# Kernel tuning notes

Measured on AMD Instinct MI355X. Metric: run time of the kernel, lower is better.

The kernel has to match this reference:

```python
import jax, jax.numpy as jnp
import numpy as np

N_NODES = 100000
N_EDGES = 800000
N_GRAPHS = 256
IN_C = 96
HID = 96
OUT_C = 16


def setup_inputs() -> dict:
    key = jax.random.key(0)
    ks = jax.random.split(key, 10)
    x = jax.random.normal(ks[0], (N_NODES, IN_C), dtype=jnp.float32)
    edge_index = jax.random.randint(ks[1], (2, N_EDGES), 0, N_NODES, dtype=jnp.int64)
    batch = jnp.sort(jax.random.randint(ks[2], (N_NODES,), 0, N_GRAPHS, dtype=jnp.int64))
    def glorot(k, fan_in, fan_out):
        s = np.sqrt(6.0 / (fan_in + fan_out)).astype(np.float32)
        return jax.random.uniform(k, (fan_in, fan_out), minval=-s, maxval=s, dtype=jnp.float32)
    W1 = glorot(ks[3], IN_C, HID)
    W2 = glorot(ks[4], HID, HID)
    W3 = glorot(ks[5], HID, HID)
    Wlin = glorot(ks[6], HID, OUT_C)
    b1 = jnp.zeros((HID,), dtype=jnp.float32)
    b2 = jnp.zeros((HID,), dtype=jnp.float32)
    b3 = jnp.zeros((HID,), dtype=jnp.float32)
    return {"x": x, "edge_index": edge_index, "batch": batch,
            "W1": W1, "b1": b1, "W2": W2, "b2": b2, "W3": W3, "b3": b3, "Wlin": Wlin}


def _gcn_conv(x, W, b, src, dst):
    # PyG GCNConv(normalize=True): add self-loops, deg includes self-loop,
    # norm_ij = deg_i^{-1/2} * deg_j^{-1/2}; linear (no bias) then scatter-add; bias after.
    n = x.shape[0]
    deg = jnp.zeros((n,), dtype=x.dtype).at[dst].add(1.0) + 1.0  # +1 self-loop
    dinv = jax.lax.rsqrt(deg)
    h = x @ W                                   # [N, H]
    coef = dinv[src] * dinv[dst]                # [E]
    msg = h[src] * coef[:, None]                # [E, H] gather
    agg = jax.ops.segment_sum(msg, dst, num_segments=n)  # scatter-add
    agg = agg + h * (dinv * dinv)[:, None]      # self-loop contribution
    return agg + b


def reference(x, edge_index, batch, W1, b1, W2, b2, W3, b3, Wlin):
    src, dst = edge_index[0], edge_index[1]
    h = jax.nn.relu(_gcn_conv(x, W1, b1, src, dst))
    h = jax.nn.relu(_gcn_conv(h, W2, b2, src, dst))
    h = _gcn_conv(h, W3, b3, src, dst)
    # global mean pool over graphs
    sums = jax.ops.segment_sum(h, batch, num_segments=N_GRAPHS)
    counts = jax.ops.segment_sum(jnp.ones((h.shape[0],), dtype=h.dtype), batch, num_segments=N_GRAPHS)
    pooled = sums / jnp.maximum(counts, 1.0)[:, None]
    return pooled @ Wlin
```

## Files before the change

kernel.cpp:

```cpp
#include <hip/hip_runtime.h>

#define NN 100000
#define NE 800000
#define NG 256
#define CH 96
#define OC 16
#define NBLK 391
#define TM 128

typedef __attribute__((ext_vector_type(8))) short bf16x8;
typedef __attribute__((ext_vector_type(4))) float f32x4;

__device__ __forceinline__ unsigned short f2bf(float x) {
    unsigned u = __float_as_uint(x);
    return (unsigned short)((u + 0x7fffu + ((u >> 16) & 1u)) >> 16);
}
__device__ __forceinline__ float bf2f(unsigned short h) {
    return __uint_as_float(((unsigned)h) << 16);
}
__device__ __forceinline__ void split8(const float4 a, const float4 b,
                                       bf16x8& hi, bf16x8& lo) {
    float v[8] = {a.x, a.y, a.z, a.w, b.x, b.y, b.z, b.w};
#pragma unroll
    for (int j = 0; j < 8; j++) {
        unsigned short h = f2bf(v[j]);
        hi[j] = (short)h;
        lo[j] = (short)f2bf(v[j] - bf2f(h));
    }
}
__device__ __forceinline__ float4 us4_to_f4(ushort4 u) {
    return make_float4(bf2f(u.x), bf2f(u.y), bf2f(u.z), bf2f(u.w));
}

__global__ __launch_bounds__(256) void k_hist(const int* __restrict__ dst,
                                              int* __restrict__ cnt,
                                              int* __restrict__ slot,
                                              const float* __restrict__ W1,
                                              const float* __restrict__ W2,
                                              const float* __restrict__ W3,
                                              unsigned short* __restrict__ WH,
                                              unsigned short* __restrict__ WL) {
    int e = blockIdx.x * 256 + threadIdx.x;
    slot[e] = atomicAdd(&cnt[dst[e]], 1);
    if (e < 3 * CH * CH) {
        int w = e / (CH * CH);
        int r = e - w * (CH * CH);
        int k = r / CH;
        int n = r - k * CH;
        const float* Ws = (w == 0) ? W1 : (w == 1) ? W2 : W3;
        float v = Ws[k * CH + n];
        unsigned short h = f2bf(v);
        WH[w * CH * CH + n * CH + k] = h;
        WL[w * CH * CH + n * CH + k] = f2bf(v - bf2f(h));
    }
}

__global__ __launch_bounds__(256) void k_offsets(const int* __restrict__ cnt,
                                                 int* __restrict__ gtot,
                                                 int* __restrict__ off,
                                                 float* __restrict__ dinv,
                                                 const int* __restrict__ batch,
                                                 int* __restrict__ goff) {
    int i = blockIdx.x * 256 + threadIdx.x;
    if (i >= NN) return;
    int c = cnt[i];
    off[i] = atomicAdd(gtot, c);
    dinv[i] = rsqrtf((float)c + 1.0f);
    int b = batch[i];
    int bp = (i > 0) ? batch[i - 1] : -1;
    for (int g = bp + 1; g <= b; g++) goff[g] = i;
    if (i == NN - 1)
        for (int g = b + 1; g <= NG; g++) goff[g] = NN;
}

__global__ __launch_bounds__(256) void k_build(const int* __restrict__ src,
                                               const int* __restrict__ dst,
                                               const int* __restrict__ off,
                                               const int* __restrict__ slot,
                                               const float* __restrict__ dinv,
                                               float2* __restrict__ packed) {
    int e = blockIdx.x * 256 + threadIdx.x;
    int s = src[e];
    int d = dst[e];
    packed[off[d] + slot[e]] = make_float2(__int_as_float(s), dinv[s] * dinv[d]);
}

__global__ __launch_bounds__(256) void k_gemm_f32(const float* __restrict__ X,
                                                  const unsigned short* __restrict__ WH,
                                                  const unsigned short* __restrict__ WL,
                                                  unsigned short* __restrict__ H) {
    __shared__ __align__(16) unsigned short WsH[CH * CH];
    __shared__ __align__(16) unsigned short WsL[CH * CH];

    const int tid = threadIdx.x;
    const int n0 = blockIdx.x * TM;

    {
        const uint4* sH = reinterpret_cast<const uint4*>(WH);
        const uint4* sL = reinterpret_cast<const uint4*>(WL);
        uint4* dH = reinterpret_cast<uint4*>(WsH);
        uint4* dL = reinterpret_cast<uint4*>(WsL);
        for (int i = tid; i < CH * CH / 8; i += 256) {
            dH[i] = sH[i];
            dL[i] = sL[i];
        }
    }
    __syncthreads();

    const int lane = tid & 63;
    const int wave = tid >> 6;
    const int lrow = lane & 15;
    const int quad = lane >> 4;

    const float4* X4 = reinterpret_cast<const float4*>(X);

    f32x4 acc[2][6];
#pragma unroll
    for (int rt = 0; rt < 2; rt++)
#pragma unroll
        for (int ct = 0; ct < 6; ct++) acc[rt][ct] = (f32x4){0.f, 0.f, 0.f, 0.f};

    int arow[2];
#pragma unroll
    for (int rt = 0; rt < 2; rt++)
        arow[rt] = min(n0 + (wave * 2 + rt) * 16 + lrow, NN - 1);

#pragma unroll
    for (int kc = 0; kc < 3; kc++) {
        bf16x8 ahi[2], alo[2];
#pragma unroll
        for (int rt = 0; rt < 2; rt++) {
            int fo = (arow[rt] * CH + kc * 32 + quad * 8) >> 2;
            split8(X4[fo], X4[fo + 1], ahi[rt], alo[rt]);
        }
#pragma unroll
        for (int ct = 0; ct < 6; ct++) {
            int bo = (ct * 16 + lrow) * CH + kc * 32 + quad * 8;
            bf16x8 bhi = *reinterpret_cast<const bf16x8*>(&WsH[bo]);
            bf16x8 blo = *reinterpret_cast<const bf16x8*>(&WsL[bo]);
#pragma unroll
            for (int rt = 0; rt < 2; rt++) {
                acc[rt][ct] = __builtin_amdgcn_mfma_f32_16x16x32_bf16(
                    alo[rt], bhi, acc[rt][ct], 0, 0, 0);
                acc[rt][ct] = __builtin_amdgcn_mfma_f32_16x16x32_bf16(
                    ahi[rt], blo, acc[rt][ct], 0, 0, 0);
                acc[rt][ct] = __builtin_amdgcn_mfma_f32_16x16x32_bf16(
                    ahi[rt], bhi, acc[rt][ct], 0, 0, 0);
            }
        }
    }

#pragma unroll
    for (int rt = 0; rt < 2; rt++) {
        int rbase = n0 + (wave * 2 + rt) * 16 + quad * 4;
#pragma unroll
        for (int ct = 0; ct < 6; ct++) {
            int col = ct * 16 + lrow;
#pragma unroll
            for (int r = 0; r < 4; r++) {
                int row = rbase + r;
                if (row < NN) H[(size_t)row * CH + col] = f2bf(acc[rt][ct][r]);
            }
        }
    }
}

__global__ __launch_bounds__(256) void k_gemm_bf16(const unsigned short* __restrict__ X,
                                                   const unsigned short* __restrict__ WH,
                                                   const unsigned short* __restrict__ WL,
                                                   unsigned short* __restrict__ H) {
    __shared__ __align__(16) unsigned short WsH[CH * CH];
    __shared__ __align__(16) unsigned short WsL[CH * CH];

    const int tid = threadIdx.x;
    const int n0 = blockIdx.x * TM;

    {
        const uint4* sH = reinterpret_cast<const uint4*>(WH);
        const uint4* sL = reinterpret_cast<const uint4*>(WL);
        uint4* dH = reinterpret_cast<uint4*>(WsH);
        uint4* dL = reinterpret_cast<uint4*>(WsL);
        for (int i = tid; i < CH * CH / 8; i += 256) {
            dH[i] = sH[i];
            dL[i] = sL[i];
        }
    }
    __syncthreads();

    const int lane = tid & 63;
    const int wave = tid >> 6;
    const int lrow = lane & 15;
    const int quad = lane >> 4;

    f32x4 acc[2][6];
#pragma unroll
    for (int rt = 0; rt < 2; rt++)
#pragma unroll
        for (int ct = 0; ct < 6; ct++) acc[rt][ct] = (f32x4){0.f, 0.f, 0.f, 0.f};

    int arow[2];
#pragma unroll
    for (int rt = 0; rt < 2; rt++)
        arow[rt] = min(n0 + (wave * 2 + rt) * 16 + lrow, NN - 1);

#pragma unroll
    for (int kc = 0; kc < 3; kc++) {
        bf16x8 ahi[2];
#pragma unroll
        for (int rt = 0; rt < 2; rt++)
            ahi[rt] = *reinterpret_cast<const bf16x8*>(
                &X[(size_t)arow[rt] * CH + kc * 32 + quad * 8]);
#pragma unroll
        for (int ct = 0; ct < 6; ct++) {
            int bo = (ct * 16 + lrow) * CH + kc * 32 + quad * 8;
            bf16x8 bhi = *reinterpret_cast<const bf16x8*>(&WsH[bo]);
            bf16x8 blo = *reinterpret_cast<const bf16x8*>(&WsL[bo]);
#pragma unroll
            for (int rt = 0; rt < 2; rt++) {
                acc[rt][ct] = __builtin_amdgcn_mfma_f32_16x16x32_bf16(
                    ahi[rt], blo, acc[rt][ct], 0, 0, 0);
                acc[rt][ct] = __builtin_amdgcn_mfma_f32_16x16x32_bf16(
                    ahi[rt], bhi, acc[rt][ct], 0, 0, 0);
            }
        }
    }

#pragma unroll
    for (int rt = 0; rt < 2; rt++) {
        int rbase = n0 + (wave * 2 + rt) * 16 + quad * 4;
#pragma unroll
        for (int ct = 0; ct < 6; ct++) {
            int col = ct * 16 + lrow;
#pragma unroll
            for (int r = 0; r < 4; r++) {
                int row = rbase + r;
                if (row < NN) H[(size_t)row * CH + col] = f2bf(acc[rt][ct][r]);
            }
        }
    }
}

template <bool RELU, bool B16OUT>
__global__ __launch_bounds__(256) void k_aggregate(const int* __restrict__ off,
                                                   const int* __restrict__ cnt,
                                                   const float2* __restrict__ packed,
                                                   const float* __restrict__ dinv,
                                                   const float* __restrict__ bias,
                                                   const unsigned short* __restrict__ H,
                                                   void* __restrict__ Bout) {
    int idx = blockIdx.x * 256 + threadIdx.x;
    int n = idx / 24;
    int c4 = idx - n * 24;
    int e0 = off[n];
    int e1 = e0 + cnt[n];

    const ushort4* H4 = reinterpret_cast<const ushort4*>(H);
    float di = dinv[n];
    float d2 = di * di;
    float4 h = us4_to_f4(H4[(size_t)n * 24 + c4]);
    float4 bb = reinterpret_cast<const float4*>(bias)[c4];
    float4 acc = make_float4(h.x * d2 + bb.x, h.y * d2 + bb.y,
                             h.z * d2 + bb.z, h.w * d2 + bb.w);

    int e = e0;
    for (; e + 4 <= e1; e += 4) {
        float2 p0 = packed[e + 0];
        float2 p1 = packed[e + 1];
        float2 p2 = packed[e + 2];
        float2 p3 = packed[e + 3];
        float4 v0 = us4_to_f4(H4[(size_t)__float_as_int(p0.x) * 24 + c4]);
        float4 v1 = us4_to_f4(H4[(size_t)__float_as_int(p1.x) * 24 + c4]);
        float4 v2 = us4_to_f4(H4[(size_t)__float_as_int(p2.x) * 24 + c4]);
        float4 v3 = us4_to_f4(H4[(size_t)__float_as_int(p3.x) * 24 + c4]);
        acc.x += v0.x * p0.y + v1.x * p1.y + v2.x * p2.y + v3.x * p3.y;
        acc.y += v0.y * p0.y + v1.y * p1.y + v2.y * p2.y + v3.y * p3.y;
        acc.z += v0.z * p0.y + v1.z * p1.y + v2.z * p2.y + v3.z * p3.y;
        acc.w += v0.w * p0.y + v1.w * p1.y + v2.w * p2.y + v3.w * p3.y;
    }
    for (; e < e1; e++) {
        float2 pc = packed[e];
        float4 v = us4_to_f4(H4[(size_t)__float_as_int(pc.x) * 24 + c4]);
        acc.x += v.x * pc.y; acc.y += v.y * pc.y;
        acc.z += v.z * pc.y; acc.w += v.w * pc.y;
    }
    if (RELU) {
        acc.x = fmaxf(acc.x, 0.0f); acc.y = fmaxf(acc.y, 0.0f);
        acc.z = fmaxf(acc.z, 0.0f); acc.w = fmaxf(acc.w, 0.0f);
    }
    if (B16OUT) {
        ushort4 o;
        o.x = f2bf(acc.x); o.y = f2bf(acc.y); o.z = f2bf(acc.z); o.w = f2bf(acc.w);
        reinterpret_cast<ushort4*>(Bout)[(size_t)n * 24 + c4] = o;
    } else {
        reinterpret_cast<float4*>(Bout)[(size_t)n * 24 + c4] = acc;
    }
}

__global__ __launch_bounds__(384) void k_pool_linear(const int* __restrict__ goff,
                                                     const float* __restrict__ B,
                                                     const float* __restrict__ Wlin,
                                                     float* __restrict__ out) {
    __shared__ float4 sh[16][24];
    __shared__ float pooled[CH];
    int g = blockIdx.x;
    int t = threadIdx.x;
    int nl = t / 24;
    int c4 = t - nl * 24;
    int s = goff[g];
    int e = goff[g + 1];

    float4 acc = make_float4(0.f, 0.f, 0.f, 0.f);
    const float4* B4 = reinterpret_cast<const float4*>(B);
    for (int n = s + nl; n < e; n += 16) {
        float4 v = B4[(size_t)n * 24 + c4];
        acc.x += v.x; acc.y += v.y; acc.z += v.z; acc.w += v.w;
    }
    sh[nl][c4] = acc;
    __syncthreads();

    if (t < 24) {
        float4 r = make_float4(0.f, 0.f, 0.f, 0.f);
#pragma unroll
        for (int j = 0; j < 16; j++) {
            float4 v = sh[j][t];
            r.x += v.x; r.y += v.y; r.z += v.z; r.w += v.w;
        }
        float inv = 1.0f / fmaxf((float)(e - s), 1.0f);
        pooled[t * 4 + 0] = r.x * inv;
        pooled[t * 4 + 1] = r.y * inv;
        pooled[t * 4 + 2] = r.z * inv;
        pooled[t * 4 + 3] = r.w * inv;
    }
    __syncthreads();

    if (t < OC) {
        float a = 0.0f;
#pragma unroll 8
        for (int k = 0; k < CH; k++) a += pooled[k] * Wlin[k * OC + t];
        out[g * OC + t] = a;
    }
}

extern "C" void kernel_launch(void* const* d_in, const int* in_sizes, int n_in,
                              void* d_out, int out_size, void* d_ws, size_t ws_size,
                              hipStream_t stream) {
    const float* x = (const float*)d_in[0];
    const int* ei = (const int*)d_in[1];
    const int* src = ei;
    const int* dst = ei + NE;
    const int* batch = (const int*)d_in[2];
    const float* W1 = (const float*)d_in[3];
    const float* b1 = (const float*)d_in[4];
    const float* W2 = (const float*)d_in[5];
    const float* b2 = (const float*)d_in[6];
    const float* W3 = (const float*)d_in[7];
    const float* b3 = (const float*)d_in[8];
    const float* Wlin = (const float*)d_in[9];
    float* out = (float*)d_out;

    char* ws = (char*)d_ws;
    unsigned short* Ha = (unsigned short*)ws;  ws += (size_t)NN * CH * 2;
    unsigned short* Hb = (unsigned short*)ws;  ws += (size_t)NN * CH * 2;
    unsigned short* Bb = (unsigned short*)ws;  ws += (size_t)NN * CH * 2;
    float* B = (float*)ws;          ws += (size_t)NN * CH * 4;
    float2* packed = (float2*)ws;   ws += (size_t)NE * 8;
    unsigned short* WH = (unsigned short*)ws;  ws += 3 * CH * CH * 2;
    unsigned short* WL = (unsigned short*)ws;  ws += 3 * CH * CH * 2;
    float* dinv = (float*)ws;       ws += NN * 4;
    int* off = (int*)ws;            ws += NN * 4;
    int* goff = (int*)ws;           ws += 272 * 4;
    int* cnt = (int*)ws;            ws += (NN + 4) * 4;
    int* gtot = cnt + NN;
    int* slot = (int*)B;

    hipMemsetAsync(cnt, 0, (NN + 4) * 4, stream);
    k_hist<<<NE / 256, 256, 0, stream>>>(dst, cnt, slot, W1, W2, W3, WH, WL);
    k_offsets<<<NBLK, 256, 0, stream>>>(cnt, gtot, off, dinv, batch, goff);
    k_build<<<NE / 256, 256, 0, stream>>>(src, dst, off, slot, dinv, packed);

    const int gblk = (NN + TM - 1) / TM;

    k_gemm_f32<<<gblk, 256, 0, stream>>>(x, WH, WL, Ha);
    k_aggregate<true, true><<<NN * 24 / 256, 256, 0, stream>>>(
        off, cnt, packed, dinv, b1, Ha, Bb);

    k_gemm_bf16<<<gblk, 256, 0, stream>>>(Bb, WH + CH * CH, WL + CH * CH, Hb);
    k_aggregate<true, true><<<NN * 24 / 256, 256, 0, stream>>>(
        off, cnt, packed, dinv, b2, Hb, Bb);

    k_gemm_bf16<<<gblk, 256, 0, stream>>>(Bb, WH + 2 * CH * CH, WL + 2 * CH * CH, Ha);
    k_aggregate<false, false><<<NN * 24 / 256, 256, 0, stream>>>(
        off, cnt, packed, dinv, b3, Ha, B);

    k_pool_linear<<<NG, 384, 0, stream>>>(goff, B, Wlin, out);
}
```

Measured before the change: 323.4 us.

## Fuse histogram into first GEMM launch, widen aggregate to 8 channels, bf16 final output

Replaces the memset and histogram kernel with an init kernel that zeroes the counters and converts the weights. A combined front kernel runs the first GEMM blocks alongside the edge-histogram blocks in one launch. The aggregate kernel now has each thread handle 8 bf16 channels through 16-byte loads, which halves the thread count and the per-thread packed-edge reads. The final layer output is stored as bf16 instead of fp32, so pooling reads half the bytes, at the cost of precision loss before the mean pool.

```diff
diff --git a/kernel.cpp b/kernel.cpp
--- a/kernel.cpp
+++ b/kernel.cpp
@@ -7,6 +7,7 @@
 #define OC 16
 #define NBLK 391
 #define TM 128
+#define GBLK 782
 
 typedef __attribute__((ext_vector_type(8))) short bf16x8;
 typedef __attribute__((ext_vector_type(4))) float f32x4;
@@ -31,20 +32,24 @@
 __device__ __forceinline__ float4 us4_to_f4(ushort4 u) {
     return make_float4(bf2f(u.x), bf2f(u.y), bf2f(u.z), bf2f(u.w));
 }
-
-__global__ __launch_bounds__(256) void k_hist(const int* __restrict__ dst,
-                                              int* __restrict__ cnt,
-                                              int* __restrict__ slot,
+__device__ __forceinline__ void unpack8(uint4 v, float* f) {
+    f[0] = __uint_as_float(v.x << 16); f[1] = __uint_as_float(v.x & 0xffff0000u);
+    f[2] = __uint_as_float(v.y << 16); f[3] = __uint_as_float(v.y & 0xffff0000u);
+    f[4] = __uint_as_float(v.z << 16); f[5] = __uint_as_float(v.z & 0xffff0000u);
+    f[6] = __uint_as_float(v.w << 16); f[7] = __uint_as_float(v.w & 0xffff0000u);
+}
+
+__global__ __launch_bounds__(256) void k_init(int* __restrict__ cnt,
                                               const float* __restrict__ W1,
                                               const float* __restrict__ W2,
                                               const float* __restrict__ W3,
                                               unsigned short* __restrict__ WH,
                                               unsigned short* __restrict__ WL) {
-    int e = blockIdx.x * 256 + threadIdx.x;
-    slot[e] = atomicAdd(&cnt[dst[e]], 1);
-    if (e < 3 * CH * CH) {
-        int w = e / (CH * CH);
-        int r = e - w * (CH * CH);
+    int id = blockIdx.x * 256 + threadIdx.x;
+    if (id < NN + 4) cnt[id] = 0;
+    if (id < 3 * CH * CH) {
+        int w = id / (CH * CH);
+        int r = id - w * (CH * CH);
         int k = r / CH;
         int n = r - k * CH;
         const float* Ws = (w == 0) ? W1 : (w == 1) ? W2 : W3;
@@ -52,6 +57,95 @@
         unsigned short h = f2bf(v);
         WH[w * CH * CH + n * CH + k] = h;
         WL[w * CH * CH + n * CH + k] = f2bf(v - bf2f(h));
+    }
+}
+
+__global__ __launch_bounds__(256) void k_front(const float* __restrict__ X,
+                                               const unsigned short* __restrict__ WH,
+                                               const unsigned short* __restrict__ WL,
+                                               unsigned short* __restrict__ H,
+                                               const int* __restrict__ dst,
+                                               int* __restrict__ cnt,
+                                               int* __restrict__ slot) {
+    __shared__ __align__(16) unsigned short WsH[CH * CH];
+    __shared__ __align__(16) unsigned short WsL[CH * CH];
+
+    const int tid = threadIdx.x;
+
+    if (blockIdx.x >= GBLK) {
+        int e = (blockIdx.x - GBLK) * 256 + tid;
+        slot[e] = atomicAdd(&cnt[dst[e]], 1);
+        return;
+    }
+
+    const int n0 = blockIdx.x * TM;
+    {
+        const uint4* sH = reinterpret_cast<const uint4*>(WH);
+        const uint4* sL = reinterpret_cast<const uint4*>(WL);
+        uint4* dH = reinterpret_cast<uint4*>(WsH);
+        uint4* dL = reinterpret_cast<uint4*>(WsL);
+        for (int i = tid; i < CH * CH / 8; i += 256) {
+            dH[i] = sH[i];
+            dL[i] = sL[i];
+        }
+    }
+    __syncthreads();
+
+    const int lane = tid & 63;
+    const int wave = tid >> 6;
+    const int lrow = lane & 15;
+    const int quad = lane >> 4;
+
+    const float4* X4 = reinterpret_cast<const float4*>(X);
+
+    f32x4 acc[2][6];
+#pragma unroll
+    for (int rt = 0; rt < 2; rt++)
+#pragma unroll
+        for (int ct = 0; ct < 6; ct++) acc[rt][ct] = (f32x4){0.f, 0.f, 0.f, 0.f};
+
+    int arow[2];
+#pragma unroll
+    for (int rt = 0; rt < 2; rt++)
+        arow[rt] = min(n0 + (wave * 2 + rt) * 16 + lrow, NN - 1);
+
+#pragma unroll
+    for (int kc = 0; kc < 3; kc++) {
+        bf16x8 ahi[2], alo[2];
+#pragma unroll
+        for (int rt = 0; rt < 2; rt++) {
+            int fo = (arow[rt] * CH + kc * 32 + quad * 8) >> 2;
+            split8(X4[fo], X4[fo + 1], ahi[rt], alo[rt]);
+        }
+#pragma unroll
+        for (int ct = 0; ct < 6; ct++) {
+            int bo = (ct * 16 + lrow) * CH + kc * 32 + quad * 8;
+            bf16x8 bhi = *reinterpret_cast<const bf16x8*>(&WsH[bo]);
+            bf16x8 blo = *reinterpret_cast<const bf16x8*>(&WsL[bo]);
+#pragma unroll
+            for (int rt = 0; rt < 2; rt++) {
+                acc[rt][ct] = __builtin_amdgcn_mfma_f32_16x16x32_bf16(
+                    alo[rt], bhi, acc[rt][ct], 0, 0, 0);
+                acc[rt][ct] = __builtin_amdgcn_mfma_f32_16x16x32_bf16(
+                    ahi[rt], blo, acc[rt][ct], 0, 0, 0);
+                acc[rt][ct] = __builtin_amdgcn_mfma_f32_16x16x32_bf16(
+                    ahi[rt], bhi, acc[rt][ct], 0, 0, 0);
+            }
+        }
+    }
+
+#pragma unroll
+    for (int rt = 0; rt < 2; rt++) {
+        int rbase = n0 + (wave * 2 + rt) * 16 + quad * 4;
+#pragma unroll
+        for (int ct = 0; ct < 6; ct++) {
+            int col = ct * 16 + lrow;
+#pragma unroll
+            for (int r = 0; r < 4; r++) {
+                int row = rbase + r;
+                if (row < NN) H[(size_t)row * CH + col] = f2bf(acc[rt][ct][r]);
+            }
+        }
     }
 }
 
@@ -85,10 +179,10 @@
     packed[off[d] + slot[e]] = make_float2(__int_as_float(s), dinv[s] * dinv[d]);
 }
 
-__global__ __launch_bounds__(256) void k_gemm_f32(const float* __restrict__ X,
-                                                  const unsigned short* __restrict__ WH,
-                                                  const unsigned short* __restrict__ WL,
-                                                  unsigned short* __restrict__ H) {
+__global__ __launch_bounds__(256) void k_gemm_bf16(const unsigned short* __restrict__ X,
+                                                   const unsigned short* __restrict__ WH,
+                                                   const unsigned short* __restrict__ WL,
+                                                   unsigned short* __restrict__ H) {
     __shared__ __align__(16) unsigned short WsH[CH * CH];
     __shared__ __align__(16) unsigned short WsL[CH * CH];
 
@@ -112,86 +206,6 @@
     const int lrow = lane & 15;
     const int quad = lane >> 4;
 
-    const float4* X4 = reinterpret_cast<const float4*>(X);
-
-    f32x4 acc[2][6];
-#pragma unroll
-    for (int rt = 0; rt < 2; rt++)
-#pragma unroll
-        for (int ct = 0; ct < 6; ct++) acc[rt][ct] = (f32x4){0.f, 0.f, 0.f, 0.f};
-
-    int arow[2];
-#pragma unroll
-    for (int rt = 0; rt < 2; rt++)
-        arow[rt] = min(n0 + (wave * 2 + rt) * 16 + lrow, NN - 1);
-
-#pragma unroll
-    for (int kc = 0; kc < 3; kc++) {
-        bf16x8 ahi[2], alo[2];
-#pragma unroll
-        for (int rt = 0; rt < 2; rt++) {
-            int fo = (arow[rt] * CH + kc * 32 + quad * 8) >> 2;
-            split8(X4[fo], X4[fo + 1], ahi[rt], alo[rt]);
-        }
-#pragma unroll
-        for (int ct = 0; ct < 6; ct++) {
-            int bo = (ct * 16 + lrow) * CH + kc * 32 + quad * 8;
-            bf16x8 bhi = *reinterpret_cast<const bf16x8*>(&WsH[bo]);
-            bf16x8 blo = *reinterpret_cast<const bf16x8*>(&WsL[bo]);
-#pragma unroll
-            for (int rt = 0; rt < 2; rt++) {
-                acc[rt][ct] = __builtin_amdgcn_mfma_f32_16x16x32_bf16(
-                    alo[rt], bhi, acc[rt][ct], 0, 0, 0);
-                acc[rt][ct] = __builtin_amdgcn_mfma_f32_16x16x32_bf16(
-                    ahi[rt], blo, acc[rt][ct], 0, 0, 0);
-                acc[rt][ct] = __builtin_amdgcn_mfma_f32_16x16x32_bf16(
-                    ahi[rt], bhi, acc[rt][ct], 0, 0, 0);
-            }
-        }
-    }
-
-#pragma unroll
-    for (int rt = 0; rt < 2; rt++) {
-        int rbase = n0 + (wave * 2 + rt) * 16 + quad * 4;
-#pragma unroll
-        for (int ct = 0; ct < 6; ct++) {
-            int col = ct * 16 + lrow;
-#pragma unroll
-            for (int r = 0; r < 4; r++) {
-                int row = rbase + r;
-                if (row < NN) H[(size_t)row * CH + col] = f2bf(acc[rt][ct][r]);
-            }
-        }
-    }
-}
-
-__global__ __launch_bounds__(256) void k_gemm_bf16(const unsigned short* __restrict__ X,
-                                                   const unsigned short* __restrict__ WH,
-                                                   const unsigned short* __restrict__ WL,
-                                                   unsigned short* __restrict__ H) {
-    __shared__ __align__(16) unsigned short WsH[CH * CH];
-    __shared__ __align__(16) unsigned short WsL[CH * CH];
-
-    const int tid = threadIdx.x;
-    const int n0 = blockIdx.x * TM;
-
-    {
-        const uint4* sH = reinterpret_cast<const uint4*>(WH);
-        const uint4* sL = reinterpret_cast<const uint4*>(WL);
-        uint4* dH = reinterpret_cast<uint4*>(WsH);
-        uint4* dL = reinterpret_cast<uint4*>(WsL);
-        for (int i = tid; i < CH * CH / 8; i += 256) {
-            dH[i] = sH[i];
-            dL[i] = sL[i];
-        }
-    }
-    __syncthreads();
-
-    const int lane = tid & 63;
-    const int wave = tid >> 6;
-    const int lrow = lane & 15;
-    const int quad = lane >> 4;
-
     f32x4 acc[2][6];
 #pragma unroll
     for (int rt = 0; rt < 2; rt++)
@@ -240,27 +254,35 @@
     }
 }
 
-template <bool RELU, bool B16OUT>
+template <bool RELU>
 __global__ __launch_bounds__(256) void k_aggregate(const int* __restrict__ off,
                                                    const int* __restrict__ cnt,
                                                    const float2* __restrict__ packed,
                                                    const float* __restrict__ dinv,
                                                    const float* __restrict__ bias,
                                                    const unsigned short* __restrict__ H,
-                                                   void* __restrict__ Bout) {
+                                                   unsigned short* __restrict__ Bout) {
     int idx = blockIdx.x * 256 + threadIdx.x;
-    int n = idx / 24;
-    int c4 = idx - n * 24;
+    if (idx >= NN * 12) return;
+    int n = idx / 12;
+    int c8 = idx - n * 12;
     int e0 = off[n];
     int e1 = e0 + cnt[n];
 
-    const ushort4* H4 = reinterpret_cast<const ushort4*>(H);
-    float di = dinv[n];
-    float d2 = di * di;
-    float4 h = us4_to_f4(H4[(size_t)n * 24 + c4]);
-    float4 bb = reinterpret_cast<const float4*>(bias)[c4];
-    float4 acc = make_float4(h.x * d2 + bb.x, h.y * d2 + bb.y,
-                             h.z * d2 + bb.z, h.w * d2 + bb.w);
+    const uint4* H8 = reinterpret_cast<const uint4*>(H);
+
+    float a[8];
+    {
+        float hf[8];
+        unpack8(H8[(size_t)n * 12 + c8], hf);
+        float di = dinv[n];
+        float d2 = di * di;
+        const float4* bias4 = reinterpret_cast<const float4*>(bias);
+        float4 b0 = bias4[c8 * 2], b1 = bias4[c8 * 2 + 1];
+        float bf[8] = {b0.x, b0.y, b0.z, b0.w, b1.x, b1.y, b1.z, b1.w};
+#pragma unroll
+        for (int j = 0; j < 8; j++) a[j] = hf[j] * d2 + bf[j];
+    }
 
     int e = e0;
     for (; e + 4 <= e1; e += 4) {
@@ -268,36 +290,38 @@
         float2 p1 = packed[e + 1];
         float2 p2 = packed[e + 2];
         float2 p3 = packed[e + 3];
-        float4 v0 = us4_to_f4(H4[(size_t)__float_as_int(p0.x) * 24 + c4]);
-        float4 v1 = us4_to_f4(H4[(size_t)__float_as_int(p1.x) * 24 + c4]);
-        float4 v2 = us4_to_f4(H4[(size_t)__float_as_int(p2.x) * 24 + c4]);
-        float4 v3 = us4_to_f4(H4[(size_t)__float_as_int(p3.x) * 24 + c4]);
-        acc.x += v0.x * p0.y + v1.x * p1.y + v2.x * p2.y + v3.x * p3.y;
-        acc.y += v0.y * p0.y + v1.y * p1.y + v2.y * p2.y + v3.y * p3.y;
-        acc.z += v0.z * p0.y + v1.z * p1.y + v2.z * p2.y + v3.z * p3.y;
-        acc.w += v0.w * p0.y + v1.w * p1.y + v2.w * p2.y + v3.w * p3.y;
+        uint4 v0 = H8[(size_t)__float_as_int(p0.x) * 12 + c8];
+        uint4 v1 = H8[(size_t)__float_as_int(p1.x) * 12 + c8];
+        uint4 v2 = H8[(size_t)__float_as_int(p2.x) * 12 + c8];
+        uint4 v3 = H8[(size_t)__float_as_int(p3.x) * 12 + c8];
+        float f0[8], f1[8], f2[8], f3[8];
+        unpack8(v0, f0); unpack8(v1, f1); unpack8(v2, f2); unpack8(v3, f3);
+#pragma unroll
+        for (int j = 0; j < 8; j++)
+            a[j] += f0[j] * p0.y + f1[j] * p1.y + f2[j] * p2.y + f3[j] * p3.y;
     }
     for (; e < e1; e++) {
         float2 pc = packed[e];
-        float4 v = us4_to_f4(H4[(size_t)__float_as_int(pc.x) * 24 + c4]);
-        acc.x += v.x * pc.y; acc.y += v.y * pc.y;
-        acc.z += v.z * pc.y; acc.w += v.w * pc.y;
+        uint4 v = H8[(size_t)__float_as_int(pc.x) * 12 + c8];
+        float f[8];
+        unpack8(v, f);
+#pragma unroll
+        for (int j = 0; j < 8; j++) a[j] += f[j] * pc.y;
     }
     if (RELU) {
-        acc.x = fmaxf(acc.x, 0.0f); acc.y = fmaxf(acc.y, 0.0f);
-        acc.z = fmaxf(acc.z, 0.0f); acc.w = fmaxf(acc.w, 0.0f);
-    }
-    if (B16OUT) {
-        ushort4 o;
-        o.x = f2bf(acc.x); o.y = f2bf(acc.y); o.z = f2bf(acc.z); o.w = f2bf(acc.w);
-        reinterpret_cast<ushort4*>(Bout)[(size_t)n * 24 + c4] = o;
-    } else {
-        reinterpret_cast<float4*>(Bout)[(size_t)n * 24 + c4] = acc;
-    }
+#pragma unroll
+        for (int j = 0; j < 8; j++) a[j] = fmaxf(a[j], 0.0f);
+    }
+    uint4 o;
+    o.x = (unsigned)f2bf(a[0]) | ((unsigned)f2bf(a[1]) << 16);
+    o.y = (unsigned)f2bf(a[2]) | ((unsigned)f2bf(a[3]) << 16);
+    o.z = (unsigned)f2bf(a[4]) | ((unsigned)f2bf(a[5]) << 16);
+    o.w = (unsigned)f2bf(a[6]) | ((unsigned)f2bf(a[7]) << 16);
+    reinterpret_cast<uint4*>(Bout)[(size_t)n * 12 + c8] = o;
 }
 
 __global__ __launch_bounds__(384) void k_pool_linear(const int* __restrict__ goff,
-                                                     const float* __restrict__ B,
+                                                     const unsigned short* __restrict__ B,
                                                      const float* __restrict__ Wlin,
                                                      float* __restrict__ out) {
     __shared__ float4 sh[16][24];
@@ -310,9 +334,9 @@
     int e = goff[g + 1];
 
     float4 acc = make_float4(0.f, 0.f, 0.f, 0.f);
-    const float4* B4 = reinterpret_cast<const float4*>(B);
+    const ushort4* B4 = reinterpret_cast<const ushort4*>(B);
     for (int n = s + nl; n < e; n += 16) {
-        float4 v = B4[(size_t)n * 24 + c4];
+        float4 v = us4_to_f4(B4[(size_t)n * 24 + c4]);
         acc.x += v.x; acc.y += v.y; acc.z += v.z; acc.w += v.w;
     }
     sh[nl][c4] = acc;
@@ -362,7 +386,6 @@
     unsigned short* Ha = (unsigned short*)ws;  ws += (size_t)NN * CH * 2;
     unsigned short* Hb = (unsigned short*)ws;  ws += (size_t)NN * CH * 2;
     unsigned short* Bb = (unsigned short*)ws;  ws += (size_t)NN * CH * 2;
-    float* B = (float*)ws;          ws += (size_t)NN * CH * 4;
     float2* packed = (float2*)ws;   ws += (size_t)NE * 8;
     unsigned short* WH = (unsigned short*)ws;  ws += 3 * CH * CH * 2;
     unsigned short* WL = (unsigned short*)ws;  ws += 3 * CH * CH * 2;
@@ -371,26 +394,20 @@
     int* goff = (int*)ws;           ws += 272 * 4;
     int* cnt = (int*)ws;            ws += (NN + 4) * 4;
     int* gtot = cnt + NN;
-    int* slot = (int*)B;
-
-    hipMemsetAsync(cnt, 0, (NN + 4) * 4, stream);
-    k_hist<<<NE / 256, 256, 0, stream>>>(dst, cnt, slot, W1, W2, W3, WH, WL);
+    int* slot = (int*)Bb;
+
+    k_init<<<NBLK, 256, 0, stream>>>(cnt, W1, W2, W3, WH, WL);
+    k_front<<<GBLK + NE / 256, 256, 0, stream>>>(x, WH, WL, Ha, dst, cnt, slot);
     k_offsets<<<NBLK, 256, 0, stream>>>(cnt, gtot, off, dinv, batch, goff);
     k_build<<<NE / 256, 256, 0, stream>>>(src, dst, off, slot, dinv, packed);
 
-    const int gblk = (NN + TM - 1) / TM;
-
-    k_gemm_f32<<<gblk, 256, 0, stream>>>(x, WH, WL, Ha);
-    k_aggregate<true, true><<<NN * 24 / 256, 256, 0, stream>>>(
-        off, cnt, packed, dinv, b1, Ha, Bb);
-
-    k_gemm_bf16<<<gblk, 256, 0, stream>>>(Bb, WH + CH * CH, WL + CH * CH, Hb);
-    k_aggregate<true, true><<<NN * 24 / 256, 256, 0, stream>>>(
-        off, cnt, packed, dinv, b2, Hb, Bb);
-
-    k_gemm_bf16<<<gblk, 256, 0, stream>>>(Bb, WH + 2 * CH * CH, WL + 2 * CH * CH, Ha);
-    k_aggregate<false, false><<<NN * 24 / 256, 256, 0, stream>>>(
-        off, cnt, packed, dinv, b3, Ha, B);
-
-    k_pool_linear<<<NG, 384, 0, stream>>>(goff, B, Wlin, out);
-}
+    const int ablk = (NN * 12 + 255) / 256;
+
+    k_aggregate<true><<<ablk, 256, 0, stream>>>(off, cnt, packed, dinv, b1, Ha, Bb);
+    k_gemm_bf16<<<GBLK, 256, 0, stream>>>(Bb, WH + CH * CH, WL + CH * CH, Hb);
+    k_aggregate<true><<<ablk, 256, 0, stream>>>(off, cnt, packed, dinv, b2, Hb, Bb);
+    k_gemm_bf16<<<GBLK, 256, 0, stream>>>(Bb, WH + 2 * CH * CH, WL + 2 * CH * CH, Ha);
+    k_aggregate<false><<<ablk, 256, 0, stream>>>(off, cnt, packed, dinv, b3, Ha, Bb);
+
+    k_pool_linear<<<NG, 384, 0, stream>>>(goff, Bb, Wlin, out);
+}
```

After: 302.0 us. 1.07x faster.
